# Kernel optimization log

Measured on AMD Instinct MI355X. Metric: run time of the kernel, lower is better.

Reference implementation:

```python
import jax, jax.numpy as jnp
import numpy as np

V, E, H = 32000, 512, 1024
B, T = 32, 64

def setup_inputs() -> dict:
    key = jax.random.key(0)
    ks = jax.random.split(key, 8)
    return {
        "x": jax.random.randint(ks[0], (B, T), 0, V, dtype=jnp.int32),
        "state_h": jax.random.normal(ks[1], (B, H), dtype=jnp.float32),
        "state_c": jax.random.normal(ks[2], (B, H), dtype=jnp.float32),
        "emb_table": jax.random.normal(ks[3], (V, E), dtype=jnp.float32) * 0.02,
        "W": jax.random.normal(ks[4], (E, 4 * H), dtype=jnp.float32) * (1.0 / np.sqrt(E)),
        "U": jax.random.normal(ks[5], (H, 4 * H), dtype=jnp.float32) * (1.0 / np.sqrt(H)),
        "b": jnp.zeros((4 * H,), dtype=jnp.float32),
        "dense_W": jax.random.normal(ks[6], (H, V), dtype=jnp.float32) * (1.0 / np.sqrt(H)),
        "dense_b": jnp.zeros((V,), dtype=jnp.float32),
    }

def _lstm(emb, h0, c0, W, U, b):
    # Precompute input projections for all timesteps: [B,T,4H]
    xW = jnp.einsum('bte,eg->btg', emb, W) + b
    def step(carry, xw_t):
        h, c = carry
        z = xw_t + h @ U  # [B,4H]
        i, f, g, o = jnp.split(z, 4, axis=-1)  # Keras gate order i,f,c,o
        i = jax.nn.sigmoid(i)
        f = jax.nn.sigmoid(f)
        g = jnp.tanh(g)
        o = jax.nn.sigmoid(o)
        c = f * c + i * g
        h = o * jnp.tanh(c)
        return (h, c), h
    (h, c), hs = jax.lax.scan(step, (h0, c0), xW.transpose(1, 0, 2))
    return hs.transpose(1, 0, 2), h, c  # [B,T,H], [B,H], [B,H]

def reference(x, state_h, state_c, emb_table, W, U, b, dense_W, dense_b):
    emb = emb_table[x]  # [B,T,E]
    seq, h, c = _lstm(emb, state_h, state_c, W, U, b)
    logits = jnp.einsum('bth,hv->btv', seq, dense_W) + dense_b  # [B,T,V]
    return logits, h, c
```

## Files before the change

kernel.cpp:

```cpp
#include <hip/hip_runtime.h>

typedef unsigned short u16;
typedef __bf16 bf16x8 __attribute__((ext_vector_type(8)));
typedef float f32x4 __attribute__((ext_vector_type(4)));
typedef u16 u16x8 __attribute__((ext_vector_type(8)));
typedef u16 u16x4 __attribute__((ext_vector_type(4)));

#define T_STEPS 64
#define BATCH 32
#define HDIM 1024
#define EDIM 512
#define VDIM 32000
#define GDIM 4096

__device__ __forceinline__ u16 f2b(float v) {
  unsigned x = __float_as_uint(v);
  return (u16)((x + 0x7fffu + ((x >> 16) & 1u)) >> 16);
}

__device__ __forceinline__ float ftanh(float x) {
  float ax = fabsf(x);
  float e = __expf(2.f * ax);
  float t = 1.f - 2.f / (e + 1.f);
  return copysignf(t, x);
}

__device__ __forceinline__ void gload16(const void* g, void* l) {
  __builtin_amdgcn_global_load_lds(
      (const __attribute__((address_space(1))) void*)g,
      (__attribute__((address_space(3))) void*)l, 16, 0, 0);
}

__device__ __forceinline__ f32x4 mfma16(bf16x8 a, bf16x8 b, f32x4 c) {
  return __builtin_amdgcn_mfma_f32_16x16x32_bf16(a, b, c, 0, 0, 0);
}


__global__ __launch_bounds__(256) void gather_init_k(
    const int* __restrict__ x, const float* __restrict__ emb,
    u16* __restrict__ A, const float* __restrict__ h0,
    const float* __restrict__ c0, u16* __restrict__ h0b,
    float* __restrict__ c_ws) {
  int tid = threadIdx.x;
  if (blockIdx.x < 1024) {
    int bt = blockIdx.x * 2 + (tid >> 7);
    int tok = x[bt];
    const float4* src = (const float4*)(emb + (size_t)tok * EDIM);
    u16x4* dst = (u16x4*)(A + (size_t)bt * EDIM);
    int i = tid & 127;
    float4 v = src[i];
    u16x4 o = {f2b(v.x), f2b(v.y), f2b(v.z), f2b(v.w)};
    dst[i] = o;
  } else {
    int i = (blockIdx.x - 1024) * 256 + tid;
    h0b[i] = f2b(h0[i]);
    c_ws[i] = c0[i];
  }
}

__global__ __launch_bounds__(256) void transpose_cvt_k(
    const float* __restrict__ in, u16* __restrict__ out, int K, int N) {
  __shared__ float tile[64][65];
  int n0 = blockIdx.x * 64, k0 = blockIdx.y * 64;
  int tid = threadIdx.x;
  int r0 = tid >> 4;
  int c4 = (tid & 15) * 4;
#pragma unroll
  for (int rr = 0; rr < 4; ++rr) {
    int r = rr * 16 + r0;
    float4 v = *reinterpret_cast<const float4*>(
        &in[(size_t)(k0 + r) * N + n0 + c4]);
    *reinterpret_cast<float4*>(&tile[r][c4]) = v;
  }
  __syncthreads();
  int wr2 = tid >> 3, c8 = (tid & 7) * 8;
#pragma unroll
  for (int rr = 0; rr < 2; ++rr) {
    int r = rr * 32 + wr2;
    u16x8 o;
#pragma unroll
    for (int k = 0; k < 8; ++k) o[k] = f2b(tile[c8 + k][r]);
    *reinterpret_cast<u16x8*>(&out[(size_t)(n0 + r) * K + k0 + c8]) = o;
  }
}

__global__ __launch_bounds__(256) void transpose_cvt_permU_k(
    const float* __restrict__ in, u16* __restrict__ out) {
  const int K = HDIM, N = GDIM;
  __shared__ float tile[64][65];
  int n0 = blockIdx.x * 64, k0 = blockIdx.y * 64;
  int tid = threadIdx.x;
  int r0 = tid >> 4;
  int c4 = (tid & 15) * 4;
#pragma unroll
  for (int rr = 0; rr < 4; ++rr) {
    int r = rr * 16 + r0;
    float4 v = *reinterpret_cast<const float4*>(
        &in[(size_t)(k0 + r) * N + n0 + c4]);
    *reinterpret_cast<float4*>(&tile[r][c4]) = v;
  }
  __syncthreads();
  int wr2 = tid >> 3, c8 = (tid & 7) * 8;
#pragma unroll
  for (int rr = 0; rr < 2; ++rr) {
    int r = rr * 32 + wr2;
    int n = n0 + r;
    int g = n >> 10, c = n & 1023;
    int pn = ((c >> 2) << 4) + (g << 2) + (c & 3);
    u16x8 o;
#pragma unroll
    for (int k = 0; k < 8; ++k) o[k] = f2b(tile[c8 + k][r]);
    *reinterpret_cast<u16x8*>(&out[(size_t)pn * K + k0 + c8]) = o;
  }
}


#define STG_A(dst, h, kb)                                              \
  do {                                                                 \
    gload16(Abytes + offA[h][0] + (kb), (dst) + (h) * 16384 + w * 1024); \
    gload16(Abytes + offA[h][1] + (kb),                                \
            (dst) + (h) * 16384 + 8192 + w * 1024);                    \
  } while (0)
#define STG_B(dst, h, kb)                                              \
  do {                                                                 \
    gload16(Bbytes + offB[h][0] + (kb),                                \
            (dst) + 32768 + (h) * 16384 + w * 1024);                   \
    gload16(Bbytes + offB[h][1] + (kb),                                \
            (dst) + 32768 + (h) * 16384 + 8192 + w * 1024);            \
  } while (0)
#define VMW4 asm volatile("s_waitcnt vmcnt(4)" ::: "memory")
#define VMW0 asm volatile("s_waitcnt vmcnt(0)" ::: "memory")

#define MFMA_BLOCK(mih)                                                   \
  do {                                                                    \
    __builtin_amdgcn_s_setprio(1);                                        \
    _Pragma("unroll") for (int u = 0; u < 4; ++u)                         \
        _Pragma("unroll") for (int v = 0; v < 4; ++v) {                   \
      acc[(mih)*4 + u][v] = mfma16(af[u][0], bfr[v][0], acc[(mih)*4 + u][v]); \
      acc[(mih)*4 + u][v] = mfma16(af[u][1], bfr[v][1], acc[(mih)*4 + u][v]); \
    }                                                                     \
    __builtin_amdgcn_s_setprio(0);                                        \
  } while (0)

#define PH_FULL(cur, mih, STG, WAIT)                                      \
  do {                                                                    \
    bf16x8 af[4][2];                                                      \
    _Pragma("unroll") for (int u = 0; u < 4; ++u) {                       \
      af[u][0] = *reinterpret_cast<const bf16x8*>((cur) +                 \
                                                  aoff[(mih)*4 + u][0]);  \
      af[u][1] = *reinterpret_cast<const bf16x8*>((cur) +                 \
                                                  aoff[(mih)*4 + u][1]);  \
    }                                                                     \
    _Pragma("unroll") for (int v = 0; v < 4; ++v) {                       \
      bfr[v][0] = *reinterpret_cast<const bf16x8*>((cur) + boff[v][0]);   \
      bfr[v][1] = *reinterpret_cast<const bf16x8*>((cur) + boff[v][1]);   \
    }                                                                     \
    STG;                                                                  \
    __builtin_amdgcn_s_barrier();                                         \
    asm volatile("s_waitcnt lgkmcnt(0)" ::: "memory");                    \
    MFMA_BLOCK(mih);                                                      \
    WAIT;                                                                 \
    __builtin_amdgcn_s_barrier();                                         \
  } while (0)

#define PH_A(cur, mih, STG, WAIT)                                         \
  do {                                                                    \
    bf16x8 af[4][2];                                                      \
    _Pragma("unroll") for (int u = 0; u < 4; ++u) {                       \
      af[u][0] = *reinterpret_cast<const bf16x8*>((cur) +                 \
                                                  aoff[(mih)*4 + u][0]);  \
      af[u][1] = *reinterpret_cast<const bf16x8*>((cur) +                 \
                                                  aoff[(mih)*4 + u][1]);  \
    }                                                                     \
    STG;                                                                  \
    __builtin_amdgcn_s_barrier();                                         \
    asm volatile("s_waitcnt lgkmcnt(0)" ::: "memory");                    \
    MFMA_BLOCK(mih);                                                      \
    WAIT;                                                                 \
    __builtin_amdgcn_s_barrier();                                         \
  } while (0)

__global__ __launch_bounds__(512, 2) void gemm256_k(
    const u16* __restrict__ A,
    const u16* __restrict__ BT,
    const float* __restrict__ bias,
    float* __restrict__ C,
    int M, int N, int K) {
  __shared__ __attribute__((aligned(1024))) char smem[131072];
  const int tid = threadIdx.x;
  const int w = tid >> 6, lane = tid & 63;
  const int lo16 = lane & 15, hi4 = lane >> 4;
  const int wr = w >> 2, wc = w & 3;

  const int cpx = gridDim.x >> 3;
  const int bid = blockIdx.x;
  const int swz = (bid & 7) * cpx + (bid >> 3);
  const int nmb = M >> 8;
  const int m0 = (swz % nmb) << 8, n0 = (swz / nmb) << 8;

  const char* Abytes = (const char*)A;
  const char* Bbytes = (const char*)BT;
  const int K2 = K * 2;

  int offA[2][2], offB[2][2];
#pragma unroll
  for (int h = 0; h < 2; ++h)
#pragma unroll
    for (int i = 0; i < 2; ++i) {
      int o = h * 16384 + (i * 512 + tid) * 16;
      int s = o >> 10, q = o & 1023;
      int qp = q ^ (((q >> 9) & 1) << 5);
      int row = ((s >> 1) << 4) + (qp >> 6);
      int colb = ((s & 1) << 6) + (qp & 63);
      offA[h][i] = (m0 + row) * K2 + colb;
      offB[h][i] = (n0 + row) * K2 + colb;
    }

  int aoff[8][2], boff[4][2];
#pragma unroll
  for (int mi = 0; mi < 8; ++mi)
#pragma unroll
    for (int kk = 0; kk < 2; ++kk) {
      int r = (mi >> 2) * 128 + wr * 64 + (mi & 3) * 16 + lo16;
      int q = (r & 15) * 64 + hi4 * 16;
      int qs = q ^ (((q >> 9) & 1) << 5);
      aoff[mi][kk] = (((r >> 4) << 1) + kk) * 1024 + qs;
    }
#pragma unroll
  for (int nj = 0; nj < 4; ++nj)
#pragma unroll
    for (int kk = 0; kk < 2; ++kk) {
      int r = (nj >> 1) * 128 + wc * 32 + (nj & 1) * 16 + lo16;
      int q = (r & 15) * 64 + hi4 * 16;
      int qs = q ^ (((q >> 9) & 1) << 5);
      boff[nj][kk] = 32768 + (((r >> 4) << 1) + kk) * 1024 + qs;
    }

  f32x4 acc[8][4] = {};
  bf16x8 bfr[4][2];
  char* const bd = smem;
  char* const bo = smem + 65536;

  STG_A(bd, 0, 0);
  STG_B(bd, 0, 0);
  STG_A(bd, 1, 0);
  STG_B(bd, 1, 0);
  STG_A(bo, 0, 128);
  STG_B(bo, 0, 128);
  VMW4;
  __builtin_amdgcn_s_barrier();

  const int NITER = K >> 7;
  for (int it = 0; it < NITER - 1; ++it) {
    const int k1 = (it * 128 + 64) * 2;
    const int k2 = (it * 128 + 128) * 2;
    const int k3 = (it * 128 + 192) * 2;
    PH_FULL(bd, 0, { STG_A(bo, 1, k1); STG_B(bo, 1, k1); }, ((void)0));
    PH_A(bd, 1, { STG_A(bd, 0, k2); STG_B(bd, 0, k2); }, VMW4);
    PH_FULL(bo, 0, { STG_A(bd, 1, k2); STG_B(bd, 1, k2); }, ((void)0));
    PH_A(bo, 1, { STG_A(bo, 0, k3); STG_B(bo, 0, k3); }, VMW4);
  }
  {
    const int k1 = ((NITER - 1) * 128 + 64) * 2;
    PH_FULL(bd, 0, { STG_A(bo, 1, k1); STG_B(bo, 1, k1); }, ((void)0));
    PH_A(bd, 1, ((void)0), VMW0);
    PH_FULL(bo, 0, ((void)0), ((void)0));
    PH_A(bo, 1, ((void)0), ((void)0));
  }

#pragma unroll
  for (int mi = 0; mi < 8; ++mi) {
    int row = m0 + (mi >> 2) * 128 + wr * 64 + (mi & 3) * 16 + hi4 * 4;
#pragma unroll
    for (int nj = 0; nj < 4; ++nj) {
      int col = n0 + (nj >> 1) * 128 + wc * 32 + (nj & 1) * 16 + lo16;
      float bv = bias ? bias[col] : 0.f;
#pragma unroll
      for (int j = 0; j < 4; ++j)
        C[(size_t)(row + j) * N + col] = acc[mi][nj][j] + bv;
    }
  }
}


__global__ __launch_bounds__(256) void lstm_step2_k(
    const float* __restrict__ xW,
    const u16* __restrict__ h_src,
    int h_stride,
    const u16* __restrict__ UT2,
    float* __restrict__ c_ws,
    u16* __restrict__ seq,
    float* __restrict__ out_hc,
    int t) {
  __shared__ float Zs[4][16][17];
  const int tid = threadIdx.x;
  const int w = tid >> 6, lane = tid & 63;
  const int lo16 = lane & 15, hi4 = lane >> 4;
  const int zt = blockIdx.x >> 1;
  const int bt = blockIdx.x & 1;

  const int bb = tid >> 2, jg = tid & 3;
  float xw0 = 0.f, xw1 = 0.f, xw2 = 0.f, xw3 = 0.f;
  if (tid < 64) {
    const float* xrow =
        xW + (size_t)((bt * 16 + bb) * T_STEPS + t) * GDIM + zt * 4 + jg;
    xw0 = xrow[0];
    xw1 = xrow[1024];
    xw2 = xrow[2048];
    xw3 = xrow[3072];
  }

  const u16* arow = h_src + (size_t)(bt * 16 + lo16) * h_stride;
  const u16* brow = UT2 + (size_t)(zt * 16 + lo16) * HDIM;

  f32x4 acc = {};
#pragma unroll
  for (int kc = 0; kc < 8; ++kc) {
    int k = w * 256 + kc * 32 + hi4 * 8;
    bf16x8 a = *reinterpret_cast<const bf16x8*>(arow + k);
    bf16x8 b = *reinterpret_cast<const bf16x8*>(brow + k);
    acc = mfma16(a, b, acc);
  }
#pragma unroll
  for (int j = 0; j < 4; ++j) Zs[w][hi4 * 4 + j][lo16] = acc[j];
  __syncthreads();

  if (tid < 64) {
    int b = bt * 16 + bb;
    int hcol = zt * 4 + jg;
    float z[4] = {xw0, xw1, xw2, xw3};
#pragma unroll
    for (int g = 0; g < 4; ++g)
#pragma unroll
      for (int ww = 0; ww < 4; ++ww) z[g] += Zs[ww][bb][g * 4 + jg];
    size_t cidx = (size_t)b * HDIM + hcol;
    float c_old = c_ws[cidx];
    float ig = 1.f / (1.f + __expf(-z[0]));
    float fg = 1.f / (1.f + __expf(-z[1]));
    float gg = ftanh(z[2]);
    float og = 1.f / (1.f + __expf(-z[3]));
    float cn = fg * c_old + ig * gg;
    float hn = og * ftanh(cn);
    c_ws[cidx] = cn;
    seq[(size_t)(b * T_STEPS + t) * HDIM + hcol] = f2b(hn);
    if (out_hc) {
      out_hc[cidx] = hn;
      out_hc[BATCH * HDIM + cidx] = cn;
    }
  }
}


extern "C" void kernel_launch(void* const* d_in, const int* in_sizes, int n_in,
                              void* d_out, int out_size, void* d_ws,
                              size_t ws_size, hipStream_t stream) {
  const int* x = (const int*)d_in[0];
  const float* state_h = (const float*)d_in[1];
  const float* state_c = (const float*)d_in[2];
  const float* emb = (const float*)d_in[3];
  const float* W = (const float*)d_in[4];
  const float* U = (const float*)d_in[5];
  const float* bvec = (const float*)d_in[6];
  const float* dW = (const float*)d_in[7];
  const float* db = (const float*)d_in[8];
  float* out = (float*)d_out;
  char* ws = (char*)d_ws;

  size_t off = 0;
  auto alloc = [&](size_t bytes) {
    void* p = ws + off;
    off += (bytes + 255) & ~(size_t)255;
    return p;
  };
  u16* A_emb = (u16*)alloc(2048ull * EDIM * 2);
  u16* WbT   = (u16*)alloc((size_t)GDIM * EDIM * 2);
  u16* UT2   = (u16*)alloc((size_t)GDIM * HDIM * 2);
  u16* DbT   = (u16*)alloc((size_t)VDIM * HDIM * 2);
  float* xW  = (float*)alloc(2048ull * GDIM * 4);
  u16* seq   = (u16*)alloc(2048ull * HDIM * 2);
  u16* h0b   = (u16*)alloc((size_t)BATCH * HDIM * 2);
  float* c_ws = (float*)alloc((size_t)BATCH * HDIM * 4);
  if (off > ws_size) return;

  gather_init_k<<<1152, 256, 0, stream>>>(x, emb, A_emb, state_h, state_c,
                                          h0b, c_ws);
  transpose_cvt_k<<<dim3(GDIM / 64, EDIM / 64), 256, 0, stream>>>(W, WbT, EDIM, GDIM);
  transpose_cvt_permU_k<<<dim3(GDIM / 64, HDIM / 64), 256, 0, stream>>>(U, UT2);
  transpose_cvt_k<<<dim3(VDIM / 64, HDIM / 64), 256, 0, stream>>>(dW, DbT, HDIM, VDIM);

  gemm256_k<<<dim3((2048 / 256) * (GDIM / 256)), 512, 0, stream>>>(
      A_emb, WbT, bvec, xW, 2048, GDIM, EDIM);

  for (int t = 0; t < T_STEPS; ++t) {
    const u16* h_src = (t == 0) ? h0b : (seq + (size_t)(t - 1) * HDIM);
    int h_stride = (t == 0) ? HDIM : T_STEPS * HDIM;
    float* outhc = (t == T_STEPS - 1) ? (out + 65536000ull) : nullptr;
    lstm_step2_k<<<512, 256, 0, stream>>>(xW, h_src, h_stride, UT2, c_ws, seq,
                                          outhc, t);
  }

  gemm256_k<<<dim3((2048 / 256) * (VDIM / 256)), 512, 0, stream>>>(
      seq, DbT, db, out, 2048, VDIM, HDIM);
}
```

Measured before the change: 649.8 us.

## Merge prep kernels and overlap dense weight transpose with LSTM steps

Three prep kernels (embedding gather/init, W transpose, U permuted transpose) become one launch, cutting launch overhead. The large dense_W transpose-and-convert is split across the 64 recurrent step launches: each step adds 125 extra blocks that each transpose one 64x64 tile (64*125 = 8000 tiles in total). This hides the transpose inside the latency-bound recurrence, which only uses 512 blocks. The risk is that the extra blocks compete for bandwidth and compute units and lengthen the critical-path step kernels.

```diff
diff --git a/kernel.cpp b/kernel.cpp
--- a/kernel.cpp
+++ b/kernel.cpp
@@ -35,15 +35,43 @@
   return __builtin_amdgcn_mfma_f32_16x16x32_bf16(a, b, c, 0, 0, 0);
 }
 
-
-__global__ __launch_bounds__(256) void gather_init_k(
+__device__ __forceinline__ void tr_tile(const float* __restrict__ in,
+                                        u16* __restrict__ out, int K, int N,
+                                        int n0, int k0, float (*tile)[65],
+                                        int tid) {
+  int r0 = tid >> 4;
+  int c4 = (tid & 15) * 4;
+#pragma unroll
+  for (int rr = 0; rr < 4; ++rr) {
+    int r = rr * 16 + r0;
+    float4 v = *reinterpret_cast<const float4*>(
+        &in[(size_t)(k0 + r) * N + n0 + c4]);
+    *reinterpret_cast<float4*>(&tile[r][c4]) = v;
+  }
+  __syncthreads();
+  int wr2 = tid >> 3, c8 = (tid & 7) * 8;
+#pragma unroll
+  for (int rr = 0; rr < 2; ++rr) {
+    int r = rr * 32 + wr2;
+    u16x8 o;
+#pragma unroll
+    for (int k = 0; k < 8; ++k) o[k] = f2b(tile[c8 + k][r]);
+    *reinterpret_cast<u16x8*>(&out[(size_t)(n0 + r) * K + k0 + c8]) = o;
+  }
+}
+
+__global__ __launch_bounds__(256) void prep_all_k(
     const int* __restrict__ x, const float* __restrict__ emb,
     u16* __restrict__ A, const float* __restrict__ h0,
     const float* __restrict__ c0, u16* __restrict__ h0b,
-    float* __restrict__ c_ws) {
-  int tid = threadIdx.x;
-  if (blockIdx.x < 1024) {
-    int bt = blockIdx.x * 2 + (tid >> 7);
+    float* __restrict__ c_ws, const float* __restrict__ W,
+    u16* __restrict__ WbT, const float* __restrict__ U,
+    u16* __restrict__ UT2) {
+  __shared__ float tile[64][65];
+  const int tid = threadIdx.x;
+  const int b = blockIdx.x;
+  if (b < 1024) {
+    int bt = b * 2 + (tid >> 7);
     int tok = x[bt];
     const float4* src = (const float4*)(emb + (size_t)tok * EDIM);
     u16x4* dst = (u16x4*)(A + (size_t)bt * EDIM);
@@ -51,66 +79,37 @@
     float4 v = src[i];
     u16x4 o = {f2b(v.x), f2b(v.y), f2b(v.z), f2b(v.w)};
     dst[i] = o;
-  } else {
-    int i = (blockIdx.x - 1024) * 256 + tid;
+  } else if (b < 1152) {
+    int i = (b - 1024) * 256 + tid;
     h0b[i] = f2b(h0[i]);
     c_ws[i] = c0[i];
-  }
-}
-
-__global__ __launch_bounds__(256) void transpose_cvt_k(
-    const float* __restrict__ in, u16* __restrict__ out, int K, int N) {
-  __shared__ float tile[64][65];
-  int n0 = blockIdx.x * 64, k0 = blockIdx.y * 64;
-  int tid = threadIdx.x;
-  int r0 = tid >> 4;
-  int c4 = (tid & 15) * 4;
-#pragma unroll
-  for (int rr = 0; rr < 4; ++rr) {
-    int r = rr * 16 + r0;
-    float4 v = *reinterpret_cast<const float4*>(
-        &in[(size_t)(k0 + r) * N + n0 + c4]);
-    *reinterpret_cast<float4*>(&tile[r][c4]) = v;
-  }
-  __syncthreads();
-  int wr2 = tid >> 3, c8 = (tid & 7) * 8;
-#pragma unroll
-  for (int rr = 0; rr < 2; ++rr) {
-    int r = rr * 32 + wr2;
-    u16x8 o;
-#pragma unroll
-    for (int k = 0; k < 8; ++k) o[k] = f2b(tile[c8 + k][r]);
-    *reinterpret_cast<u16x8*>(&out[(size_t)(n0 + r) * K + k0 + c8]) = o;
-  }
-}
-
-__global__ __launch_bounds__(256) void transpose_cvt_permU_k(
-    const float* __restrict__ in, u16* __restrict__ out) {
-  const int K = HDIM, N = GDIM;
-  __shared__ float tile[64][65];
-  int n0 = blockIdx.x * 64, k0 = blockIdx.y * 64;
-  int tid = threadIdx.x;
-  int r0 = tid >> 4;
-  int c4 = (tid & 15) * 4;
-#pragma unroll
-  for (int rr = 0; rr < 4; ++rr) {
-    int r = rr * 16 + r0;
-    float4 v = *reinterpret_cast<const float4*>(
-        &in[(size_t)(k0 + r) * N + n0 + c4]);
-    *reinterpret_cast<float4*>(&tile[r][c4]) = v;
-  }
-  __syncthreads();
-  int wr2 = tid >> 3, c8 = (tid & 7) * 8;
-#pragma unroll
-  for (int rr = 0; rr < 2; ++rr) {
-    int r = rr * 32 + wr2;
-    int n = n0 + r;
-    int g = n >> 10, c = n & 1023;
-    int pn = ((c >> 2) << 4) + (g << 2) + (c & 3);
-    u16x8 o;
-#pragma unroll
-    for (int k = 0; k < 8; ++k) o[k] = f2b(tile[c8 + k][r]);
-    *reinterpret_cast<u16x8*>(&out[(size_t)pn * K + k0 + c8]) = o;
+  } else if (b < 1664) {
+    int idx = b - 1152;
+    tr_tile(W, WbT, EDIM, GDIM, (idx & 63) * 64, (idx >> 6) * 64, tile, tid);
+  } else {
+    int idx = b - 1664;
+    int n0 = (idx & 63) * 64, k0 = (idx >> 6) * 64;
+    int r0 = tid >> 4, c4 = (tid & 15) * 4;
+#pragma unroll
+    for (int rr = 0; rr < 4; ++rr) {
+      int r = rr * 16 + r0;
+      float4 v = *reinterpret_cast<const float4*>(
+          &U[(size_t)(k0 + r) * GDIM + n0 + c4]);
+      *reinterpret_cast<float4*>(&tile[r][c4]) = v;
+    }
+    __syncthreads();
+    int wr2 = tid >> 3, c8 = (tid & 7) * 8;
+#pragma unroll
+    for (int rr = 0; rr < 2; ++rr) {
+      int r = rr * 32 + wr2;
+      int n = n0 + r;
+      int g = n >> 10, c = n & 1023;
+      int pn = ((c >> 2) << 4) + (g << 2) + (c & 3);
+      u16x8 o;
+#pragma unroll
+      for (int k = 0; k < 8; ++k) o[k] = f2b(tile[c8 + k][r]);
+      *reinterpret_cast<u16x8*>(&UT2[(size_t)pn * HDIM + k0 + c8]) = o;
+    }
   }
 }
 
@@ -283,7 +282,7 @@
 }
 
 
-__global__ __launch_bounds__(256) void lstm_step2_k(
+__global__ __launch_bounds__(256) void lstm_step_dbt_k(
     const float* __restrict__ xW,
     const u16* __restrict__ h_src,
     int h_stride,
@@ -291,9 +290,21 @@
     float* __restrict__ c_ws,
     u16* __restrict__ seq,
     float* __restrict__ out_hc,
+    const float* __restrict__ dW,
+    u16* __restrict__ DbT,
     int t) {
-  __shared__ float Zs[4][16][17];
+  __shared__ __align__(16) float sh[64 * 65];
   const int tid = threadIdx.x;
+
+  if (blockIdx.x >= 512) {
+    int tau = t * 125 + (int)blockIdx.x - 512;
+    int bx = tau % 500, by = tau / 500;
+    tr_tile(dW, DbT, HDIM, VDIM, bx * 64, by * 64,
+            reinterpret_cast<float(*)[65]>(sh), tid);
+    return;
+  }
+
+  float* Zs = sh;
   const int w = tid >> 6, lane = tid & 63;
   const int lo16 = lane & 15, hi4 = lane >> 4;
   const int zt = blockIdx.x >> 1;
@@ -322,7 +333,8 @@
     acc = mfma16(a, b, acc);
   }
 #pragma unroll
-  for (int j = 0; j < 4; ++j) Zs[w][hi4 * 4 + j][lo16] = acc[j];
+  for (int j = 0; j < 4; ++j)
+    Zs[w * 272 + (hi4 * 4 + j) * 17 + lo16] = acc[j];
   __syncthreads();
 
   if (tid < 64) {
@@ -332,7 +344,8 @@
 #pragma unroll
     for (int g = 0; g < 4; ++g)
 #pragma unroll
-      for (int ww = 0; ww < 4; ++ww) z[g] += Zs[ww][bb][g * 4 + jg];
+      for (int ww = 0; ww < 4; ++ww)
+        z[g] += Zs[ww * 272 + bb * 17 + g * 4 + jg];
     size_t cidx = (size_t)b * HDIM + hcol;
     float c_old = c_ws[cidx];
     float ig = 1.f / (1.f + __expf(-z[0]));
@@ -382,11 +395,8 @@
   float* c_ws = (float*)alloc((size_t)BATCH * HDIM * 4);
   if (off > ws_size) return;
 
-  gather_init_k<<<1152, 256, 0, stream>>>(x, emb, A_emb, state_h, state_c,
-                                          h0b, c_ws);
-  transpose_cvt_k<<<dim3(GDIM / 64, EDIM / 64), 256, 0, stream>>>(W, WbT, EDIM, GDIM);
-  transpose_cvt_permU_k<<<dim3(GDIM / 64, HDIM / 64), 256, 0, stream>>>(U, UT2);
-  transpose_cvt_k<<<dim3(VDIM / 64, HDIM / 64), 256, 0, stream>>>(dW, DbT, HDIM, VDIM);
+  prep_all_k<<<2688, 256, 0, stream>>>(x, emb, A_emb, state_h, state_c, h0b,
+                                       c_ws, W, WbT, U, UT2);
 
   gemm256_k<<<dim3((2048 / 256) * (GDIM / 256)), 512, 0, stream>>>(
       A_emb, WbT, bvec, xW, 2048, GDIM, EDIM);
@@ -395,8 +405,8 @@
     const u16* h_src = (t == 0) ? h0b : (seq + (size_t)(t - 1) * HDIM);
     int h_stride = (t == 0) ? HDIM : T_STEPS * HDIM;
     float* outhc = (t == T_STEPS - 1) ? (out + 65536000ull) : nullptr;
-    lstm_step2_k<<<512, 256, 0, stream>>>(xW, h_src, h_stride, UT2, c_ws, seq,
-                                          outhc, t);
+    lstm_step_dbt_k<<<637, 256, 0, stream>>>(xW, h_src, h_stride, UT2, c_ws,
+                                             seq, outhc, dW, DbT, t);
   }
 
   gemm256_k<<<dim3((2048 / 256) * (VDIM / 256)), 512, 0, stream>>>(
```

New measurement: 650.1 us. About the same (+0.0%).
